# Kernel optimization log

Hardware: AMD Instinct MI355X
Metric: run time of the kernel (lower is better)

The kernel has to match this reference:

```python
import jax, jax.numpy as jnp
import numpy as np

B, C, T, F = 2, 256, 1024, 64
N, HID = 4, 64


def setup_inputs() -> dict:
    key = jax.random.key(0)
    ks = jax.random.split(key, 9)
    s = 0.02
    return {
        "x": jax.random.normal(ks[0], (B, C, T, F), dtype=jnp.float32),
        "Wq": jax.random.normal(ks[1], (N, HID, C), dtype=jnp.float32) * s,
        "bq": jnp.zeros((N, HID), dtype=jnp.float32),
        "Wk": jax.random.normal(ks[2], (N, HID, C), dtype=jnp.float32) * s,
        "bk": jnp.zeros((N, HID), dtype=jnp.float32),
        "Wv": jax.random.normal(ks[3], (N, C // N, C), dtype=jnp.float32) * s,
        "bv": jnp.zeros((N, C // N), dtype=jnp.float32),
        "Wp": jax.random.normal(ks[4], (C, C), dtype=jnp.float32) * s,
        "bp": jnp.zeros((C,), dtype=jnp.float32),
    }


def reference(x, Wq, bq, Wk, bk, Wv, bv, Wp, bp):
    b, c, t, f = x.shape
    n = Wq.shape[0]
    # conv1x1 per head then torch: cat(dim=0) -> [N*b, h, t, f]; transpose(1,2); flatten -> [N*b, t, h*f]
    def proj(W, bias):
        h = W.shape[1]
        y = jnp.einsum('bctf,nhc->nbthf', x, W) + bias[:, None, None, :, None]
        return y.reshape(n * b, t, h * f)

    Q = proj(Wq, bq)                       # [N*b, t, hid*f]
    K = proj(Wk, bk)                       # [N*b, t, hid*f]
    V = proj(Wv, bv)                       # [N*b, t, (c/N)*f]

    scale = 1.0 / jnp.sqrt(jnp.asarray(Q.shape[-1], dtype=x.dtype))
    attn = jax.nn.softmax(jnp.einsum('mte,mse->mts', Q, K) * scale, axis=2)
    Vo = jnp.einsum('mts,msd->mtd', attn, V)             # [N*b, t, c*f/N]

    # torch: reshape(b*N, t, c*f//N).transpose(1,2).view(N,b,c//N,t,f).transpose(0,1).view(b,c,t,f)
    Vo = Vo.transpose(0, 2, 1)                            # [N*b, c*f/N, t]
    Vo = Vo.reshape(n, b, c // n, t, f)
    Vo = jnp.swapaxes(Vo, 0, 1).reshape(b, c, t, f)

    out = jnp.einsum('bctf,oc->botf', Vo, Wp) + bp[None, :, None, None]
    return out + x
```

## Files before the change

### kernel.cpp

```cpp
#include <hip/hip_runtime.h>

#define DI __device__ __forceinline__

static constexpr int B_ = 2;
static constexpr int C_ = 256;
static constexpr int T_ = 1024;
static constexpr int F_ = 64;
static constexpr int M_ = 8;
static constexpr int E_ = 4096;
static constexpr float SCALE_ = 1.0f / 64.0f;

typedef __attribute__((ext_vector_type(8))) short bf16x8;
typedef __attribute__((ext_vector_type(4))) float f32x4;

DI unsigned short bf16_rne(float f) {
    unsigned int u = __float_as_uint(f);
    return (unsigned short)((u + 0x7FFFu + ((u >> 16) & 1u)) >> 16);
}
DI float bf2f(unsigned short h) { return __uint_as_float(((unsigned int)h) << 16); }
DI ushort4 pack4(float a, float b, float c, float d) {
    return make_ushort4(bf16_rne(a), bf16_rne(b), bf16_rne(c), bf16_rne(d));
}
DI float4 up4(ushort4 u) {
    return make_float4(bf2f(u.x), bf2f(u.y), bf2f(u.z), bf2f(u.w));
}

DI void gload_lds16(const unsigned short* g, unsigned short* l) {
    __builtin_amdgcn_global_load_lds(
        (const __attribute__((address_space(1))) unsigned int*)g,
        (__attribute__((address_space(3))) unsigned int*)l, 16, 0, 0);
}

DI void mfma16(f32x4& acc, bf16x8 a, bf16x8 b) {
    asm("v_mfma_f32_16x16x32_bf16 %0, %1, %2, %0" : "+v"(acc) : "v"(a), "v"(b));
}

__global__ __launch_bounds__(256) void wconv_kernel(
    const float* __restrict__ Wq, const float* __restrict__ Wk,
    const float* __restrict__ Wv, const float* __restrict__ Wp,
    const float* __restrict__ bq, const float* __restrict__ bk,
    const float* __restrict__ bv,
    unsigned short* __restrict__ Wall, unsigned short* __restrict__ Wpb,
    float* __restrict__ bias_all)
{
    const int tid = (int)threadIdx.x;
    const int bid = (int)blockIdx.x;
    if (bid < 192) {
        const int idx = (bid * 256 + tid) * 4;
        const int proj = idx >> 16, rem = idx & 65535;
        const float* src = proj == 0 ? Wq : (proj == 1 ? Wk : Wv);
        float4 v = *(const float4*)(src + rem);
        *(ushort4*)(Wall + idx) = pack4(v.x, v.y, v.z, v.w);
        const int gid = bid * 256 + tid;
        if (gid < 768) {
            float bb = gid < 256 ? bq[gid] : (gid < 512 ? bk[gid - 256] : bv[gid - 512]);
            bias_all[gid] = bb;
        }
    } else {
        const int idx = ((bid - 192) * 256 + tid) * 4;
        float4 v = *(const float4*)(Wp + idx);
        *(ushort4*)(Wpb + idx) = pack4(v.x, v.y, v.z, v.w);
    }
}

__global__ __launch_bounds__(256) void xt_kernel(
    const float* __restrict__ x, unsigned short* __restrict__ xT)
{
    const int tf0 = blockIdx.x * 64;
    const int c0  = blockIdx.y * 64;
    const int b   = blockIdx.z;
    const int tid = (int)threadIdx.x;
    __shared__ unsigned short ts[64][68];

    const float* xb = x + (size_t)(b * 256 + c0) * 65536 + tf0;
#pragma unroll
    for (int it = 0; it < 4; ++it) {
        int idx = it * 256 + tid;
        int cl = idx >> 4, tf4 = (idx & 15) * 4;
        float4 v = *(const float4*)(xb + (size_t)cl * 65536 + tf4);
        *(ushort4*)&ts[cl][tf4] = pack4(v.x, v.y, v.z, v.w);
    }
    __syncthreads();
    const int tfl = tid >> 2, c16 = (tid & 3) * 16;
    unsigned short* op = xT + ((size_t)b * 65536 + tf0 + tfl) * 256 + c0 + c16;
#pragma unroll
    for (int q = 0; q < 4; ++q) {
        int cl = c16 + q * 4;
        ushort4 v = make_ushort4(ts[cl][tfl], ts[cl+1][tfl], ts[cl+2][tfl], ts[cl+3][tfl]);
        *(ushort4*)(op + q * 4) = v;
    }
}

__global__ __launch_bounds__(256) void qkv_fused(
    const unsigned short* __restrict__ xT, const unsigned short* __restrict__ Wall,
    const float* __restrict__ bias_all, unsigned short* __restrict__ outQ,
    int ntile_off, int nb_n, int proj_base)
{
    const int wgid = (int)blockIdx.x;
    const int b = wgid >> 9, tft = wgid & 511;
    const int tfbase = tft * 128;

    const int tid = (int)threadIdx.x;
    const int wid = tid >> 6, lane = tid & 63;
    const int wr = wid >> 1, wc = wid & 1;
    const int lo16 = lane & 15, hi4 = lane >> 4;

    __shared__ unsigned short As[4 * 128 * 64];
    __shared__ unsigned short Bs[128 * 64];

    const unsigned short* arow = xT + ((size_t)b * 65536 + tfbase) * 256;

    const int srow = lane >> 3;
    const int scol = ((lane & 7) ^ srow) * 8;

#pragma unroll
    for (int kc = 0; kc < 4; ++kc)
#pragma unroll
        for (int i = 0; i < 4; ++i) {
            const int rb = wid * 32 + i * 8;
            gload_lds16(arow + (size_t)(rb + srow) * 256 + kc * 64 + scol,
                        &As[kc * 8192 + rb * 64]);
        }

    const int tf0 = tfbase + wr * 64;
    for (int ntl = 0; ntl < nb_n; ++ntl) {
        const int nbase = (ntile_off + ntl) * 128;
        const unsigned short* brow = Wall + (size_t)nbase * 256;
        f32x4 acc[4][4] = {};

        for (int kc = 0; kc < 4; ++kc) {
#pragma unroll
            for (int i = 0; i < 4; ++i) {
                const int rb = wid * 32 + i * 8;
                gload_lds16(brow + (size_t)(rb + srow) * 256 + kc * 64 + scol,
                            &Bs[rb * 64]);
            }
            __syncthreads();
#pragma unroll
            for (int kk = 0; kk < 2; ++kk) {
                const int hc = (kk * 32 + hi4 * 8) ^ ((lane & 7) << 3);
                bf16x8 a[4], bb[4];
#pragma unroll
                for (int mi = 0; mi < 4; ++mi)
                    a[mi] = *(const bf16x8*)&As[kc * 8192 + (wr * 64 + mi * 16 + lo16) * 64 + hc];
#pragma unroll
                for (int nj = 0; nj < 4; ++nj)
                    bb[nj] = *(const bf16x8*)&Bs[(wc * 64 + nj * 16 + lo16) * 64 + hc];
#pragma unroll
                for (int mi = 0; mi < 4; ++mi)
#pragma unroll
                    for (int nj = 0; nj < 4; ++nj)
                        mfma16(acc[mi][nj], a[mi], bb[nj]);
            }
            __syncthreads();
        }

        asm volatile("s_nop 7\n\ts_nop 7" ::: "memory");
#pragma unroll
        for (int nj = 0; nj < 4; ++nj) {
            const int r_col = nbase + wc * 64 + nj * 16 + lo16;
            const int projl = (r_col >> 8) - proj_base;
            const int rr = r_col & 255;
            const int mrow = (rr >> 6) * 2 + b;
            const int h = rr & 63;
            const float bv = bias_all[r_col];
            unsigned short* dst0 = outQ + (size_t)projl * 33554432
                                 + (size_t)mrow * (T_ * E_) + h * 64;
#pragma unroll
            for (int mi = 0; mi < 4; ++mi) {
                const int tf = tf0 + mi * 16 + hi4 * 4;
                const int t = tf >> 6, f = tf & 63;
                *(ushort4*)(dst0 + (size_t)t * E_ + f) =
                    pack4(acc[mi][nj][0] + bv, acc[mi][nj][1] + bv,
                          acc[mi][nj][2] + bv, acc[mi][nj][3] + bv);
            }
        }
    }
}

__global__ __launch_bounds__(256) void scores_mfma(
    const unsigned short* __restrict__ Q, const unsigned short* __restrict__ K,
    unsigned short* __restrict__ S)
{
    const int m = blockIdx.z;
    const int tbase = blockIdx.y * 128;
    const int sbase = blockIdx.x * 128;
    const int tid = (int)threadIdx.x;
    const int wid = tid >> 6, lane = tid & 63;
    const int wr = wid >> 1, wc = wid & 1;
    const int lo16 = lane & 15, hi4 = lane >> 4;

    __shared__ unsigned short As[128 * 64];
    __shared__ unsigned short Bs[128 * 64];

    f32x4 acc[4][4] = {};

    const unsigned short* qrow = Q + ((size_t)m * T_ + tbase) * E_;
    const unsigned short* krow = K + ((size_t)m * T_ + sbase) * E_;

    const int srow = lane >> 3;
    const int scol = ((lane & 7) ^ srow) * 8;

    for (int eb = 0; eb < E_; eb += 64) {
#pragma unroll
        for (int i = 0; i < 4; ++i) {
            const int rb = wid * 32 + i * 8;
            gload_lds16(qrow + (size_t)(rb + srow) * E_ + eb + scol, &As[rb * 64]);
            gload_lds16(krow + (size_t)(rb + srow) * E_ + eb + scol, &Bs[rb * 64]);
        }
        __syncthreads();
#pragma unroll
        for (int kk = 0; kk < 2; ++kk) {
            const int hc = (kk * 32 + hi4 * 8) ^ ((lane & 7) << 3);
            bf16x8 a[4], bb[4];
#pragma unroll
            for (int mi = 0; mi < 4; ++mi)
                a[mi] = *(const bf16x8*)&As[(wr * 64 + mi * 16 + lo16) * 64 + hc];
#pragma unroll
            for (int nj = 0; nj < 4; ++nj)
                bb[nj] = *(const bf16x8*)&Bs[(wc * 64 + nj * 16 + lo16) * 64 + hc];
#pragma unroll
            for (int mi = 0; mi < 4; ++mi)
#pragma unroll
                for (int nj = 0; nj < 4; ++nj)
                    mfma16(acc[mi][nj], a[mi], bb[nj]);
        }
        __syncthreads();
    }

    asm volatile("s_nop 7\n\ts_nop 7" ::: "memory");
#pragma unroll
    for (int mi = 0; mi < 4; ++mi)
#pragma unroll
        for (int r = 0; r < 4; ++r) {
            int trow = tbase + wr * 64 + mi * 16 + hi4 * 4 + r;
            unsigned short* sp = S + ((size_t)m * T_ + trow) * T_ + sbase + wc * 64 + lo16;
#pragma unroll
            for (int nj = 0; nj < 4; ++nj)
                sp[nj * 16] = bf16_rne(acc[mi][nj][r] * SCALE_);
        }
}

__global__ __launch_bounds__(256) void softmax_kernel(
    const unsigned short* __restrict__ S, unsigned short* __restrict__ A)
{
    const size_t rowoff = ((size_t)blockIdx.y * T_ + blockIdx.x) * T_;
    const int tid = (int)threadIdx.x;
    const int wid = tid >> 6, lane = tid & 63;

    __shared__ float redmx[4];
    __shared__ float redsm[4];

    float4 v = up4(*(const ushort4*)(S + rowoff + tid * 4));
    float mx = fmaxf(fmaxf(v.x, v.y), fmaxf(v.z, v.w));
#pragma unroll
    for (int off = 32; off > 0; off >>= 1) mx = fmaxf(mx, __shfl_xor(mx, off));
    if (lane == 0) redmx[wid] = mx;
    __syncthreads();
    mx = fmaxf(fmaxf(redmx[0], redmx[1]), fmaxf(redmx[2], redmx[3]));

    float e0 = __expf(v.x - mx), e1 = __expf(v.y - mx);
    float e2 = __expf(v.z - mx), e3 = __expf(v.w - mx);
    float sm = (e0 + e1) + (e2 + e3);
#pragma unroll
    for (int off = 32; off > 0; off >>= 1) sm += __shfl_xor(sm, off);
    if (lane == 0) redsm[wid] = sm;
    __syncthreads();
    sm = (redsm[0] + redsm[1]) + (redsm[2] + redsm[3]);
    float inv = 1.0f / sm;
    *(ushort4*)(A + rowoff + tid * 4) = pack4(e0 * inv, e1 * inv, e2 * inv, e3 * inv);
}

__global__ __launch_bounds__(256) void vt_kernel(
    const unsigned short* __restrict__ V, unsigned short* __restrict__ Vt)
{
    const int m = blockIdx.z;
    const int d0 = blockIdx.x * 64;
    const int s0 = blockIdx.y * 64;
    const int tid = (int)threadIdx.x;
    __shared__ unsigned short ts[64][68];

    const unsigned short* vp = V + (size_t)m * T_ * E_;
#pragma unroll
    for (int it = 0; it < 4; ++it) {
        int idx = it * 256 + tid;
        int sl = idx >> 4, d4 = (idx & 15) * 4;
        *(ushort4*)&ts[sl][d4] = *(const ushort4*)&vp[(size_t)(s0 + sl) * E_ + d0 + d4];
    }
    __syncthreads();
    unsigned short* op = Vt + (size_t)m * E_ * T_;
    const int dl = tid >> 2, s16 = (tid & 3) * 16;
#pragma unroll
    for (int q = 0; q < 4; ++q) {
        int s4 = s16 + q * 4;
        ushort4 v = make_ushort4(ts[s4][dl], ts[s4+1][dl], ts[s4+2][dl], ts[s4+3][dl]);
        *(ushort4*)&op[(size_t)(d0 + dl) * T_ + s0 + s4] = v;
    }
}

__global__ __launch_bounds__(256) void pv_mfma(
    const unsigned short* __restrict__ A, const unsigned short* __restrict__ Vt,
    unsigned short* __restrict__ G)
{
    const int m = blockIdx.z;
    const int nh = m >> 1, b = m & 1;
    const int tbase = blockIdx.y * 128;
    const int dbase = blockIdx.x * 128;
    const int tid = (int)threadIdx.x;
    const int wid = tid >> 6, lane = tid & 63;
    const int wr = wid >> 1, wc = wid & 1;
    const int lo16 = lane & 15, hi4 = lane >> 4;

    __shared__ unsigned short As[128 * 64];
    __shared__ unsigned short Bs[128 * 64];

    f32x4 acc[4][4] = {};

    const unsigned short* arow = A  + ((size_t)m * T_ + tbase) * T_;
    const unsigned short* vrow = Vt + (size_t)m * E_ * T_ + (size_t)dbase * T_;

    const int srow = lane >> 3;
    const int scol = ((lane & 7) ^ srow) * 8;

    for (int sb = 0; sb < T_; sb += 64) {
#pragma unroll
        for (int i = 0; i < 4; ++i) {
            const int rb = wid * 32 + i * 8;
            gload_lds16(arow + (size_t)(rb + srow) * T_ + sb + scol, &As[rb * 64]);
            gload_lds16(vrow + (size_t)(rb + srow) * T_ + sb + scol, &Bs[rb * 64]);
        }
        __syncthreads();
#pragma unroll
        for (int kk = 0; kk < 2; ++kk) {
            const int hc = (kk * 32 + hi4 * 8) ^ ((lane & 7) << 3);
            bf16x8 a[4], bb[4];
#pragma unroll
            for (int mi = 0; mi < 4; ++mi)
                a[mi] = *(const bf16x8*)&As[(wr * 64 + mi * 16 + lo16) * 64 + hc];
#pragma unroll
            for (int nj = 0; nj < 4; ++nj)
                bb[nj] = *(const bf16x8*)&Bs[(wc * 64 + nj * 16 + lo16) * 64 + hc];
#pragma unroll
            for (int mi = 0; mi < 4; ++mi)
#pragma unroll
                for (int nj = 0; nj < 4; ++nj)
                    mfma16(acc[mi][nj], a[mi], bb[nj]);
        }
        __syncthreads();
    }

    asm volatile("s_nop 7\n\ts_nop 7" ::: "memory");
    const int cb   = nh * 64 + (dbase >> 6) + wc;
    const int t2lo = (tbase >> 6) + wr;
#pragma unroll
    for (int mi = 0; mi < 4; ++mi) {
        const int tl = mi * 16 + hi4 * 4;
#pragma unroll
        for (int nj = 0; nj < 4; ++nj) {
            const int d63 = nj * 16 + lo16;
            size_t addr = (((size_t)(b * 256 + cb)) * 1024 + d63 * 16 + t2lo) * 64 + tl;
            *(ushort4*)&G[addr] = pack4(acc[mi][nj][0], acc[mi][nj][1],
                                        acc[mi][nj][2], acc[mi][nj][3]);
        }
    }
}

__global__ __launch_bounds__(256) void gt_kernel(
    const unsigned short* __restrict__ G, unsigned short* __restrict__ GT)
{
    const int tf0 = blockIdx.x * 64;
    const int c0  = blockIdx.y * 64;
    const int b   = blockIdx.z;
    const int tid = (int)threadIdx.x;
    __shared__ unsigned short ts[64][68];

    const unsigned short* gb = G + (size_t)(b * 256 + c0) * 65536 + tf0;
#pragma unroll
    for (int it = 0; it < 4; ++it) {
        int idx = it * 256 + tid;
        int cl = idx >> 4, tf4 = (idx & 15) * 4;
        *(ushort4*)&ts[cl][tf4] = *(const ushort4*)(gb + (size_t)cl * 65536 + tf4);
    }
    __syncthreads();
    const int tfl = tid >> 2, c16 = (tid & 3) * 16;
    unsigned short* op = GT + ((size_t)b * 65536 + tf0 + tfl) * 256 + c0 + c16;
#pragma unroll
    for (int q = 0; q < 4; ++q) {
        int cl = c16 + q * 4;
        ushort4 v = make_ushort4(ts[cl][tfl], ts[cl+1][tfl], ts[cl+2][tfl], ts[cl+3][tfl]);
        *(ushort4*)(op + q * 4) = v;
    }
}

__global__ __launch_bounds__(256) void outproj_mfma(
    const unsigned short* __restrict__ GT, const unsigned short* __restrict__ Wpb,
    const float* __restrict__ bp, const float* __restrict__ x,
    float* __restrict__ out)
{
    const int tfbase = blockIdx.x * 128;
    const int obase  = blockIdx.y * 128;
    const int b      = blockIdx.z;
    const int tid = (int)threadIdx.x;
    const int wid = tid >> 6, lane = tid & 63;
    const int wr = wid >> 1, wc = wid & 1;
    const int lo16 = lane & 15, hi4 = lane >> 4;

    __shared__ unsigned short As[128 * 64];
    __shared__ unsigned short Bs[128 * 64];

    f32x4 acc[4][4] = {};

    const unsigned short* arow = GT + ((size_t)b * 65536 + tfbase) * 256;
    const unsigned short* brow = Wpb + (size_t)obase * 256;

    const int srow = lane >> 3;
    const int scol = ((lane & 7) ^ srow) * 8;

    for (int cb = 0; cb < 256; cb += 64) {
#pragma unroll
        for (int i = 0; i < 4; ++i) {
            const int rb = wid * 32 + i * 8;
            gload_lds16(arow + (size_t)(rb + srow) * 256 + cb + scol, &As[rb * 64]);
            gload_lds16(brow + (size_t)(rb + srow) * 256 + cb + scol, &Bs[rb * 64]);
        }
        __syncthreads();
#pragma unroll
        for (int kk = 0; kk < 2; ++kk) {
            const int hc = (kk * 32 + hi4 * 8) ^ ((lane & 7) << 3);
            bf16x8 a[4], bb[4];
#pragma unroll
            for (int mi = 0; mi < 4; ++mi)
                a[mi] = *(const bf16x8*)&As[(wr * 64 + mi * 16 + lo16) * 64 + hc];
#pragma unroll
            for (int nj = 0; nj < 4; ++nj)
                bb[nj] = *(const bf16x8*)&Bs[(wc * 64 + nj * 16 + lo16) * 64 + hc];
#pragma unroll
            for (int mi = 0; mi < 4; ++mi)
#pragma unroll
                for (int nj = 0; nj < 4; ++nj)
                    mfma16(acc[mi][nj], a[mi], bb[nj]);
        }
        __syncthreads();
    }

    asm volatile("s_nop 7\n\ts_nop 7" ::: "memory");
#pragma unroll
    for (int nj = 0; nj < 4; ++nj) {
        const int o = obase + wc * 64 + nj * 16 + lo16;
        const float bias = bp[o];
        const size_t rowb = ((size_t)(b * 256 + o)) * 65536;
#pragma unroll
        for (int mi = 0; mi < 4; ++mi) {
            const int tf = tfbase + wr * 64 + mi * 16 + hi4 * 4;
            float4 xv = *(const float4*)(x + rowb + tf);
            float4 r = make_float4(acc[mi][nj][0] + bias + xv.x,
                                   acc[mi][nj][1] + bias + xv.y,
                                   acc[mi][nj][2] + bias + xv.z,
                                   acc[mi][nj][3] + bias + xv.w);
            *(float4*)(out + rowb + tf) = r;
        }
    }
}

extern "C" void kernel_launch(void* const* d_in, const int* in_sizes, int n_in,
                              void* d_out, int out_size, void* d_ws, size_t ws_size,
                              hipStream_t stream) {
    const float* x  = (const float*)d_in[0];
    const float* Wq = (const float*)d_in[1];
    const float* bq = (const float*)d_in[2];
    const float* Wk = (const float*)d_in[3];
    const float* bk = (const float*)d_in[4];
    const float* Wv = (const float*)d_in[5];
    const float* bv = (const float*)d_in[6];
    const float* Wp = (const float*)d_in[7];
    const float* bp = (const float*)d_in[8];
    float* out = (float*)d_out;

    char* ws = (char*)d_ws;
    unsigned short* Q    = (unsigned short*)(ws);
    unsigned short* K    = (unsigned short*)(ws + 67108864);
    unsigned short* xT   = (unsigned short*)(ws + 134217728);
    unsigned short* S    = (unsigned short*)(ws + 201326592);
    unsigned short* A    = (unsigned short*)(ws + 218103808);
    unsigned short* Wall = (unsigned short*)(ws + 234881024);
    float* bias_all      = (float*)(ws + 235274240);
    unsigned short* Wpb  = (unsigned short*)(ws + 235277312);
    unsigned short* V  = Q;
    unsigned short* Vt = K;
    unsigned short* G  = xT;
    unsigned short* GT = Q;

    wconv_kernel<<<256, 256, 0, stream>>>(Wq, Wk, Wv, Wp, bq, bk, bv, Wall, Wpb, bias_all);
    xt_kernel<<<dim3(1024, 4, 2), 256, 0, stream>>>(x, xT);
    qkv_fused<<<1024, 256, 0, stream>>>(xT, Wall, bias_all, Q, 0, 4, 0);
    scores_mfma<<<dim3(8, 8, M_), 256, 0, stream>>>(Q, K, S);
    qkv_fused<<<1024, 256, 0, stream>>>(xT, Wall, bias_all, V, 4, 2, 2);
    softmax_kernel<<<dim3(T_, M_), 256, 0, stream>>>(S, A);
    vt_kernel<<<dim3(64, 16, M_), 256, 0, stream>>>(V, Vt);
    pv_mfma<<<dim3(32, 8, M_), 256, 0, stream>>>(A, Vt, G);
    gt_kernel<<<dim3(1024, 4, 2), 256, 0, stream>>>(G, GT);
    outproj_mfma<<<dim3(512, 2, 2), 256, 0, stream>>>(GT, Wpb, bp, x, out);
}
```

Baseline: 431.7 us.

## Fuse x transpose into single QKV projection kernel and remap GEMM workgroups

Removes the separate x transpose/bf16 conversion kernel: the QKV projection now reads fp32 x directly, converts and swizzles it into LDS, and computes all Q, K, V tiles in one launch. V gets its own workspace buffer so it no longer aliases Q. The scores and PV GEMMs switch to 1D grids with a remapped workgroup index that interleaves heads across consecutive blocks, likely to spread work across XCDs and improve cache locality. The cost is strided fp32 global reads in the projection prologue and a longer-running fused kernel.

New measurement: 409.5 us. 5.1% less time.

```diff
diff --git a/kernel.cpp b/kernel.cpp
--- a/kernel.cpp
+++ b/kernel.cpp
@@ -63,38 +63,9 @@
     }
 }
 
-__global__ __launch_bounds__(256) void xt_kernel(
-    const float* __restrict__ x, unsigned short* __restrict__ xT)
-{
-    const int tf0 = blockIdx.x * 64;
-    const int c0  = blockIdx.y * 64;
-    const int b   = blockIdx.z;
-    const int tid = (int)threadIdx.x;
-    __shared__ unsigned short ts[64][68];
-
-    const float* xb = x + (size_t)(b * 256 + c0) * 65536 + tf0;
-#pragma unroll
-    for (int it = 0; it < 4; ++it) {
-        int idx = it * 256 + tid;
-        int cl = idx >> 4, tf4 = (idx & 15) * 4;
-        float4 v = *(const float4*)(xb + (size_t)cl * 65536 + tf4);
-        *(ushort4*)&ts[cl][tf4] = pack4(v.x, v.y, v.z, v.w);
-    }
-    __syncthreads();
-    const int tfl = tid >> 2, c16 = (tid & 3) * 16;
-    unsigned short* op = xT + ((size_t)b * 65536 + tf0 + tfl) * 256 + c0 + c16;
-#pragma unroll
-    for (int q = 0; q < 4; ++q) {
-        int cl = c16 + q * 4;
-        ushort4 v = make_ushort4(ts[cl][tfl], ts[cl+1][tfl], ts[cl+2][tfl], ts[cl+3][tfl]);
-        *(ushort4*)(op + q * 4) = v;
-    }
-}
-
-__global__ __launch_bounds__(256) void qkv_fused(
-    const unsigned short* __restrict__ xT, const unsigned short* __restrict__ Wall,
-    const float* __restrict__ bias_all, unsigned short* __restrict__ outQ,
-    int ntile_off, int nb_n, int proj_base)
+__global__ __launch_bounds__(256) void qkv_one(
+    const float* __restrict__ x, const unsigned short* __restrict__ Wall,
+    const float* __restrict__ bias_all, unsigned short* __restrict__ outQ)
 {
     const int wgid = (int)blockIdx.x;
     const int b = wgid >> 9, tft = wgid & 511;
@@ -108,23 +79,41 @@
     __shared__ unsigned short As[4 * 128 * 64];
     __shared__ unsigned short Bs[128 * 64];
 
-    const unsigned short* arow = xT + ((size_t)b * 65536 + tfbase) * 256;
+    {
+        const int a = lane & 7, cg = lane >> 3;
+        const int rowb = wid * 32 + a * 4;
+        const float* xb = x + (size_t)b * (C_ * T_ * F_) + tfbase + rowb;
+        for (int cb = 0; cb < 256; cb += 64) {
+            const int c0 = cb + cg * 8;
+            float4 v[8];
+#pragma unroll
+            for (int g = 0; g < 8; ++g)
+                v[g] = *(const float4*)(xb + (size_t)(c0 + g) * 65536);
+            const int kc = cb >> 6;
+#pragma unroll
+            for (int j = 0; j < 4; ++j) {
+                const int row = rowb + j;
+                const int col8 = cg ^ (row & 7);
+                ushort4 lo = pack4(v[0].x + 0.f, v[1].x, v[2].x, v[3].x);
+                float e0 = (&v[0].x)[j], e1 = (&v[1].x)[j], e2 = (&v[2].x)[j], e3 = (&v[3].x)[j];
+                float e4 = (&v[4].x)[j], e5 = (&v[5].x)[j], e6 = (&v[6].x)[j], e7 = (&v[7].x)[j];
+                ushort4 p0 = pack4(e0, e1, e2, e3);
+                ushort4 p1 = pack4(e4, e5, e6, e7);
+                (void)lo;
+                *(ushort4*)&As[kc * 8192 + row * 64 + col8 * 8]     = p0;
+                *(ushort4*)&As[kc * 8192 + row * 64 + col8 * 8 + 4] = p1;
+            }
+        }
+    }
 
     const int srow = lane >> 3;
     const int scol = ((lane & 7) ^ srow) * 8;
-
-#pragma unroll
-    for (int kc = 0; kc < 4; ++kc)
-#pragma unroll
-        for (int i = 0; i < 4; ++i) {
-            const int rb = wid * 32 + i * 8;
-            gload_lds16(arow + (size_t)(rb + srow) * 256 + kc * 64 + scol,
-                        &As[kc * 8192 + rb * 64]);
-        }
-
     const int tf0 = tfbase + wr * 64;
-    for (int ntl = 0; ntl < nb_n; ++ntl) {
-        const int nbase = (ntile_off + ntl) * 128;
+
+    __syncthreads();
+
+    for (int ntl = 0; ntl < 6; ++ntl) {
+        const int nbase = ntl * 128;
         const unsigned short* brow = Wall + (size_t)nbase * 256;
         f32x4 acc[4][4] = {};
 
@@ -159,7 +148,7 @@
 #pragma unroll
         for (int nj = 0; nj < 4; ++nj) {
             const int r_col = nbase + wc * 64 + nj * 16 + lo16;
-            const int projl = (r_col >> 8) - proj_base;
+            const int projl = r_col >> 8;
             const int rr = r_col & 255;
             const int mrow = (rr >> 6) * 2 + b;
             const int h = rr & 63;
@@ -175,6 +164,7 @@
                           acc[mi][nj][2] + bv, acc[mi][nj][3] + bv);
             }
         }
+        if (ntl < 5) __syncthreads();
     }
 }
 
@@ -182,9 +172,12 @@
     const unsigned short* __restrict__ Q, const unsigned short* __restrict__ K,
     unsigned short* __restrict__ S)
 {
-    const int m = blockIdx.z;
-    const int tbase = blockIdx.y * 128;
-    const int sbase = blockIdx.x * 128;
+    const int orig = (int)blockIdx.x;
+    const int wg = (orig & 7) * 64 + (orig >> 3);
+    const int m = wg >> 6;
+    const int rest = wg & 63;
+    const int sbase = (rest & 7) * 128;
+    const int tbase = (rest >> 3) * 128;
     const int tid = (int)threadIdx.x;
     const int wid = tid >> 6, lane = tid & 63;
     const int wr = wid >> 1, wc = wid & 1;
@@ -302,10 +295,13 @@
     const unsigned short* __restrict__ A, const unsigned short* __restrict__ Vt,
     unsigned short* __restrict__ G)
 {
-    const int m = blockIdx.z;
+    const int orig = (int)blockIdx.x;
+    const int wg = (orig & 7) * 256 + (orig >> 3);
+    const int m = wg >> 8;
+    const int rest = wg & 255;
+    const int dbase = (rest & 31) * 128;
+    const int tbase = (rest >> 5) * 128;
     const int nh = m >> 1, b = m & 1;
-    const int tbase = blockIdx.y * 128;
-    const int dbase = blockIdx.x * 128;
     const int tid = (int)threadIdx.x;
     const int wid = tid >> 6, lane = tid & 63;
     const int wr = wid >> 1, wc = wid & 1;
@@ -479,25 +475,22 @@
     char* ws = (char*)d_ws;
     unsigned short* Q    = (unsigned short*)(ws);
     unsigned short* K    = (unsigned short*)(ws + 67108864);
-    unsigned short* xT   = (unsigned short*)(ws + 134217728);
+    unsigned short* V    = (unsigned short*)(ws + 134217728);
     unsigned short* S    = (unsigned short*)(ws + 201326592);
     unsigned short* A    = (unsigned short*)(ws + 218103808);
     unsigned short* Wall = (unsigned short*)(ws + 234881024);
     float* bias_all      = (float*)(ws + 235274240);
     unsigned short* Wpb  = (unsigned short*)(ws + 235277312);
-    unsigned short* V  = Q;
     unsigned short* Vt = K;
-    unsigned short* G  = xT;
-    unsigned short* GT = Q;
+    unsigned short* G  = Q;
+    unsigned short* GT = V;
 
     wconv_kernel<<<256, 256, 0, stream>>>(Wq, Wk, Wv, Wp, bq, bk, bv, Wall, Wpb, bias_all);
-    xt_kernel<<<dim3(1024, 4, 2), 256, 0, stream>>>(x, xT);
-    qkv_fused<<<1024, 256, 0, stream>>>(xT, Wall, bias_all, Q, 0, 4, 0);
-    scores_mfma<<<dim3(8, 8, M_), 256, 0, stream>>>(Q, K, S);
-    qkv_fused<<<1024, 256, 0, stream>>>(xT, Wall, bias_all, V, 4, 2, 2);
+    qkv_one<<<1024, 256, 0, stream>>>(x, Wall, bias_all, Q);
+    scores_mfma<<<512, 256, 0, stream>>>(Q, K, S);
     softmax_kernel<<<dim3(T_, M_), 256, 0, stream>>>(S, A);
     vt_kernel<<<dim3(64, 16, M_), 256, 0, stream>>>(V, Vt);
-    pv_mfma<<<dim3(32, 8, M_), 256, 0, stream>>>(A, Vt, G);
+    pv_mfma<<<2048, 256, 0, stream>>>(A, Vt, G);
     gt_kernel<<<dim3(1024, 4, 2), 256, 0, stream>>>(G, GT);
     outproj_mfma<<<dim3(512, 2, 2), 256, 0, stream>>>(GT, Wpb, bp, x, out);
 }
```
